# Kernel tuning notes

Measured on AMD Instinct MI355X. Metric: run time of the kernel, lower is better.

The kernel has to match this reference:

```python
import jax, jax.numpy as jnp
import numpy as np

N_NODES = 50000
N_EDGES = 800000
DIM = 256
DEPTH = 4
N_REL = 4
EPS = 1e-5


def setup_inputs() -> dict:
    key = jax.random.key(0)
    ks = jax.random.split(key, 8)
    scale = 1.0 / np.sqrt(DIM)
    return {
        "node_embedding": jax.random.normal(ks[0], (N_NODES, DIM), jnp.float32),
        "weights": jax.random.normal(ks[1], (DEPTH, N_REL, DIM, DIM), jnp.float32) * scale,
        "roots": jax.random.normal(ks[2], (DEPTH, DIM, DIM), jnp.float32) * scale,
        "biases": jax.random.normal(ks[3], (DEPTH, DIM), jnp.float32) * 0.01,
        "ln_gamma": jnp.ones((DEPTH, DIM), jnp.float32),
        "ln_beta": jnp.zeros((DEPTH, DIM), jnp.float32),
        "edge_index": jax.random.randint(ks[4], (2, N_EDGES), 0, N_NODES, jnp.int32),
        "edge_type": jax.random.randint(ks[5], (N_EDGES,), 0, N_REL, jnp.int32),
    }


def _rgcn_layer(X, W, root, bias, gamma, beta, src, dst, etype, inv_deg):
    # RGCNConv with aggr='mean': per-relation transform, then per-relation mean
    # over incoming edges at the target node, summed across relations.
    h = jnp.einsum('ni,rio->rno', X, W)            # [R, N, D]
    msg = h[etype, src] * inv_deg[:, None]         # [E, D] gather + per-relation 1/deg
    agg = jax.ops.segment_sum(msg, dst, num_segments=X.shape[0])  # [N, D]
    out = agg + X @ root + bias
    # LayerNorm
    mu = jnp.mean(out, axis=-1, keepdims=True)
    var = jnp.mean(jnp.square(out - mu), axis=-1, keepdims=True)
    out = (out - mu) * jax.lax.rsqrt(var + EPS) * gamma + beta
    out = jax.nn.elu(out)
    return out + X  # residual connection (dropout p=0 -> identity)


def reference(node_embedding, weights, roots, biases, ln_gamma, ln_beta, edge_index, edge_type):
    src, dst = edge_index[0], edge_index[1]
    # per-(node, relation) in-degree for the relation-wise mean aggregation
    cnt = jnp.zeros((node_embedding.shape[0], N_REL), node_embedding.dtype)
    cnt = cnt.at[dst, edge_type].add(1.0)
    inv_deg = 1.0 / jnp.maximum(cnt[dst, edge_type], 1.0)  # [E]
    X = node_embedding
    for l in range(DEPTH):
        X = _rgcn_layer(X, weights[l], roots[l], biases[l], ln_gamma[l], ln_beta[l],
                        src, dst, edge_type, inv_deg)
    return X
```

## Files before the change

kernel.cpp:

```cpp
#include <hip/hip_runtime.h>
#include <hip/hip_bf16.h>
#include <stdint.h>

#define NN 50000
#define NE 800000
#define DD 256
#define NL 4
#define NRL 4
#define KT 1280
#define KA 1024

typedef float f32x4 __attribute__((ext_vector_type(4)));
typedef __bf16 bf16x8 __attribute__((ext_vector_type(8)));
typedef __bf16 bf16x4 __attribute__((ext_vector_type(4)));
typedef unsigned short u16x4 __attribute__((ext_vector_type(4)));

static __device__ __forceinline__ unsigned short f2bf(float f) {
  __bf16 h = (__bf16)f;
  return __builtin_bit_cast(unsigned short, h);
}

static __device__ __forceinline__ u16x4 pk4(f32x4 v) {
  u16x4 o;
  o.x = f2bf(v.x); o.y = f2bf(v.y); o.z = f2bf(v.z); o.w = f2bf(v.w);
  return o;
}

static __device__ __forceinline__ void async16(const void* g, void* l) {
  __builtin_amdgcn_global_load_lds(
      (const __attribute__((address_space(1))) unsigned int*)g,
      (__attribute__((address_space(3))) unsigned int*)l, 16, 0, 0);
}

static __device__ __forceinline__ void async16nt(const void* g, void* l) {
  __builtin_amdgcn_global_load_lds(
      (const __attribute__((address_space(1))) unsigned int*)g,
      (__attribute__((address_space(3))) unsigned int*)l, 16, 0, 2);
}


__global__ __launch_bounds__(256) void k_hist(const int* __restrict__ ei,
                                              const int* __restrict__ et,
                                              int* __restrict__ cntNR) {
  int e = blockIdx.x * 256 + threadIdx.x;
  if (e >= NE) return;
  int dst = ei[NE + e];
  int r = et[e];
  atomicAdd(&cntNR[dst * 4 + r], 1);
}

__global__ __launch_bounds__(256) void k_scan1(const int* __restrict__ cntNR,
                                               int* __restrict__ offs,
                                               int* __restrict__ bsum) {
  __shared__ int sd[256];
  const int t = threadIdx.x;
  const int n = blockIdx.x * 256 + t;
  int deg = 0;
  if (n < NN) {
    const int* c = cntNR + n * 4;
    deg = c[0] + c[1] + c[2] + c[3];
  }
  sd[t] = deg;
  __syncthreads();
  int val = deg;
  for (int d = 1; d < 256; d <<= 1) {
    int other = (t >= d) ? sd[t - d] : 0;
    __syncthreads();
    val += other;
    sd[t] = val;
    __syncthreads();
  }
  if (n < NN) offs[n] = val - deg;
  if (t == 255) bsum[blockIdx.x] = val;
}

__global__ __launch_bounds__(256) void k_scan2(const int* __restrict__ bsum,
                                               int* __restrict__ boff, int nb) {
  __shared__ int sd[256];
  const int t = threadIdx.x;
  int v = (t < nb) ? bsum[t] : 0;
  sd[t] = v;
  __syncthreads();
  int val = v;
  for (int d = 1; d < 256; d <<= 1) {
    int other = (t >= d) ? sd[t - d] : 0;
    __syncthreads();
    val += other;
    sd[t] = val;
    __syncthreads();
  }
  boff[t] = val - v;
}

__global__ __launch_bounds__(256) void k_scan3(int* __restrict__ offs,
                                               const int* __restrict__ boff,
                                               int* __restrict__ cursor) {
  int n = blockIdx.x * 256 + threadIdx.x;
  if (n < NN) {
    int o = offs[n] + boff[blockIdx.x];
    offs[n] = o;
    cursor[n] = o;
  }
  if (n == 0) offs[NN] = NE;
}

__global__ __launch_bounds__(256) void k_scatter(const int* __restrict__ ei,
                                                 const int* __restrict__ et,
                                                 int* __restrict__ cursor,
                                                 uint32_t* __restrict__ packed) {
  int e = blockIdx.x * 256 + threadIdx.x;
  if (e >= NE) return;
  int src = ei[e];
  int dst = ei[NE + e];
  int r = et[e];
  int pos = atomicAdd(&cursor[dst], 1);
  packed[pos] = (uint32_t)src | ((uint32_t)r << 16);
}

__global__ __launch_bounds__(256) void k_wconv(const float* __restrict__ weights,
                                               const float* __restrict__ roots,
                                               __hip_bfloat16* __restrict__ WbigT) {
  int idx = blockIdx.x * 256 + threadIdx.x;
  if (idx >= NL * DD * KT) return;
  int l = idx / (DD * KT);
  int rem = idx - l * (DD * KT);
  int o = rem / KT;
  int k = rem - o * KT;
  float v;
  if (k < NRL * DD) {
    int r = k >> 8, i = k & 255;
    v = weights[(((size_t)(l * NRL + r) * DD) + i) * DD + o];
  } else {
    int i = k - NRL * DD;
    v = roots[((size_t)l * DD + i) * DD + o];
  }
  WbigT[idx] = __float2bfloat16(v);
}

__global__ __launch_bounds__(256) void k_cast(const float* __restrict__ X,
                                              __hip_bfloat16* __restrict__ Xbf) {
  int i = blockIdx.x * 256 + threadIdx.x;
  if (i >= NN * 64) return;
  const f32x4* Xv = (const f32x4*)X;
  ((u16x4*)Xbf)[i] = pk4(Xv[i]);
}


__global__ __launch_bounds__(256) void k_agg(const __hip_bfloat16* __restrict__ Xbf,
                                             const uint32_t* __restrict__ packed,
                                             const int* __restrict__ offs,
                                             const int* __restrict__ cntNR,
                                             __hip_bfloat16* __restrict__ Abig) {
  const int wid = (blockIdx.x * 256 + threadIdx.x) >> 6;
  const int lane = threadIdx.x & 63;
  if (wid >= NN) return;
  const int beg = offs[wid];
  const int end = offs[wid + 1];
  const bf16x4* __restrict__ Xv = (const bf16x4*)Xbf;

  f32x4 a0 = {0.f, 0.f, 0.f, 0.f}, a1 = a0, a2 = a0, a3 = a0;

  for (int e = beg; e < end; e += 8) {
    uint32_t pv[8];
    bf16x4 vv[8];
#pragma unroll
    for (int i = 0; i < 8; ++i) {
      int ee = e + i;
      ee = (ee < end) ? ee : (end - 1);
      pv[i] = packed[ee];
    }
#pragma unroll
    for (int i = 0; i < 8; ++i) {
      vv[i] = Xv[(int)(pv[i] & 0xFFFFu) * 64 + lane];
    }
    const int nv = end - e;
#pragma unroll
    for (int i = 0; i < 8; ++i) {
      if (i < nv) {
        int r = (int)(pv[i] >> 16);
        f32x4 v = {(float)vv[i][0], (float)vv[i][1], (float)vv[i][2], (float)vv[i][3]};
        if (r == 0) a0 += v;
        else if (r == 1) a1 += v;
        else if (r == 2) a2 += v;
        else a3 += v;
      }
    }
  }

  const int* c = cntNR + wid * 4;
  int c0 = c[0], c1 = c[1], c2 = c[2], c3 = c[3];
  float s0 = 1.0f / (float)(c0 > 1 ? c0 : 1);
  float s1 = 1.0f / (float)(c1 > 1 ? c1 : 1);
  float s2 = 1.0f / (float)(c2 > 1 ? c2 : 1);
  float s3 = 1.0f / (float)(c3 > 1 ? c3 : 1);

  u16x4* Arow = (u16x4*)(Abig + (size_t)wid * KA);
  __builtin_nontemporal_store(pk4(a0 * s0), Arow + 0 * 64 + lane);
  __builtin_nontemporal_store(pk4(a1 * s1), Arow + 1 * 64 + lane);
  __builtin_nontemporal_store(pk4(a2 * s2), Arow + 2 * 64 + lane);
  __builtin_nontemporal_store(pk4(a3 * s3), Arow + 3 * 64 + lane);
}


#define GBUF 20480
#define NTILE 40

__global__ __launch_bounds__(256, 2) void k_gemm(const __hip_bfloat16* __restrict__ A,
                                                 const __hip_bfloat16* __restrict__ Xbf_in,
                                                 const __hip_bfloat16* __restrict__ Bt,
                                                 const float* __restrict__ bias,
                                                 const float* __restrict__ gamma,
                                                 const float* __restrict__ beta,
                                                 const float* __restrict__ Xin,
                                                 float* __restrict__ Xout,
                                                 __hip_bfloat16* __restrict__ Xbf_out) {
  __shared__ __align__(16) char sLDS[3 * GBUF];
  __shared__ float sRed[64][4];

  const int tid = threadIdx.x;
  const int w = tid >> 6;
  const int lane = tid & 63;
  const int wm = w >> 1, wn = w & 1;
  const int quad = lane >> 4, l15 = lane & 15;
  const int mBase = blockIdx.x * 64;

  const int srow = lane >> 2;
  const int kc = (lane & 3) ^ ((srow >> 1) & 3);

  int am = mBase + w * 16 + srow;
  if (am >= NN) am = NN - 1;
  const char* agp = (const char*)A + (size_t)am * (KA * 2) + kc * 16;
  const char* agx = (const char*)Xbf_in + (size_t)am * (DD * 2) + kc * 16;
  const char* bgp0 = (const char*)Bt + (size_t)(w * 64 + 0 + srow) * (KT * 2) + kc * 16;
  const char* bgp1 = (const char*)Bt + (size_t)(w * 64 + 16 + srow) * (KT * 2) + kc * 16;
  const char* bgp2 = (const char*)Bt + (size_t)(w * 64 + 32 + srow) * (KT * 2) + kc * 16;
  const char* bgp3 = (const char*)Bt + (size_t)(w * 64 + 48 + srow) * (KT * 2) + kc * 16;

  char* const lA = sLDS + w * 1024;
  char* const lB = sLDS + 4096 + w * 4096;

  f32x4 acc[2][8];
#pragma unroll
  for (int i = 0; i < 2; ++i)
#pragma unroll
    for (int j = 0; j < 8; ++j) acc[i][j] = (f32x4){0.f, 0.f, 0.f, 0.f};

  const int aslot = (quad ^ ((l15 >> 1) & 3)) * 16;
  const char* const aBase = sLDS + (wm * 32 + l15) * 64 + aslot;
  const char* const bBase = sLDS + 4096 + (wn * 128 + l15) * 64 + aslot;

  auto STAGE = [&](int buf, int ts) {
    const int k0 = ts * 64;
    char* la = lA + buf * GBUF;
    char* lb = lB + buf * GBUF;
    if (k0 < KA * 2) {
      async16nt(agp + k0, la);
    } else {
      async16(agx + (k0 - KA * 2), la);
    }
    async16(bgp0 + k0, lb);
    async16(bgp1 + k0, lb + 1024);
    async16(bgp2 + k0, lb + 2048);
    async16(bgp3 + k0, lb + 3072);
  };

  STAGE(0, 0);
  int cb = 0, sb = 1;
  for (int t = 0; t < NTILE; ++t) {
    const int ts = (t + 1 < NTILE) ? (t + 1) : (NTILE - 1);
    STAGE(sb, ts);
    __builtin_amdgcn_sched_barrier(0);
    asm volatile("s_waitcnt vmcnt(5)" ::: "memory");
    __builtin_amdgcn_s_barrier();
    __builtin_amdgcn_sched_barrier(0);

    const char* aAddr = aBase + cb * GBUF;
    const char* bAddr = bBase + cb * GBUF;
    bf16x8 a0 = *(const bf16x8*)(aAddr + 0 * 1024);
    bf16x8 a1 = *(const bf16x8*)(aAddr + 1 * 1024);
#pragma unroll
    for (int nt = 0; nt < 8; ++nt) {
      bf16x8 b = *(const bf16x8*)(bAddr + nt * 1024);
      acc[0][nt] = __builtin_amdgcn_mfma_f32_16x16x32_bf16(a0, b, acc[0][nt], 0, 0, 0);
      acc[1][nt] = __builtin_amdgcn_mfma_f32_16x16x32_bf16(a1, b, acc[1][nt], 0, 0, 0);
    }
    cb = (cb == 2) ? 0 : cb + 1;
    sb = (sb == 2) ? 0 : sb + 1;
  }

  float bv[8], gv[8], bev[8];
#pragma unroll
  for (int nt = 0; nt < 8; ++nt) {
    int n = wn * 128 + nt * 16 + l15;
    bv[nt] = bias[n];
    gv[nt] = gamma[n];
    bev[nt] = beta[n];
  }

#pragma unroll
  for (int mt = 0; mt < 2; ++mt) {
#pragma unroll
    for (int reg = 0; reg < 4; ++reg) {
      float s = 0.f, q = 0.f;
#pragma unroll
      for (int nt = 0; nt < 8; ++nt) {
        float v = acc[mt][nt][reg] + bv[nt];
        acc[mt][nt][reg] = v;
        s += v;
        q += v * v;
      }
#pragma unroll
      for (int d = 1; d < 16; d <<= 1) {
        s += __shfl_xor(s, d, 64);
        q += __shfl_xor(q, d, 64);
      }
      if (l15 == 0) {
        int row = wm * 32 + mt * 16 + quad * 4 + reg;
        sRed[row][wn * 2] = s;
        sRed[row][wn * 2 + 1] = q;
      }
    }
  }
  __syncthreads();

#pragma unroll
  for (int mt = 0; mt < 2; ++mt) {
#pragma unroll
    for (int reg = 0; reg < 4; ++reg) {
      int row = wm * 32 + mt * 16 + quad * 4 + reg;
      float ts = sRed[row][0] + sRed[row][2];
      float tq = sRed[row][1] + sRed[row][3];
      float mean = ts * (1.0f / 256.0f);
      float var = tq * (1.0f / 256.0f) - mean * mean;
      float rstd = rsqrtf(var + 1e-5f);
      int m = mBase + row;
      if (m < NN) {
#pragma unroll
        for (int nt = 0; nt < 8; ++nt) {
          int n = wn * 128 + nt * 16 + l15;
          float v = (acc[mt][nt][reg] - mean) * rstd * gv[nt] + bev[nt];
          v = v > 0.0f ? v : (__expf(v) - 1.0f);
          float res = v + Xin[(size_t)m * 256 + n];
          Xout[(size_t)m * 256 + n] = res;
          Xbf_out[(size_t)m * 256 + n] = __float2bfloat16(res);
        }
      }
    }
  }
}


extern "C" void kernel_launch(void* const* d_in, const int* in_sizes, int n_in,
                              void* d_out, int out_size, void* d_ws, size_t ws_size,
                              hipStream_t stream) {
  const float* X0 = (const float*)d_in[0];
  const float* weights = (const float*)d_in[1];
  const float* roots = (const float*)d_in[2];
  const float* biases = (const float*)d_in[3];
  const float* ln_g = (const float*)d_in[4];
  const float* ln_b = (const float*)d_in[5];
  const int* eidx = (const int*)d_in[6];
  const int* etyp = (const int*)d_in[7];
  float* out = (float*)d_out;

  char* ws = (char*)d_ws;
  size_t off = 0;
  auto alloc = [&](size_t bytes) -> char* {
    char* p = ws + off;
    off = (off + bytes + 255) & ~(size_t)255;
    return p;
  };
  __hip_bfloat16* Abig = (__hip_bfloat16*)alloc((size_t)NN * KA * 2);
  __hip_bfloat16* WbigT = (__hip_bfloat16*)alloc((size_t)NL * DD * KT * 2);
  float* Xb0 = (float*)alloc((size_t)NN * DD * 4);
  float* Xb1 = (float*)alloc((size_t)NN * DD * 4);
  __hip_bfloat16* Xbf0 = (__hip_bfloat16*)alloc((size_t)NN * DD * 2);
  __hip_bfloat16* Xbf1 = (__hip_bfloat16*)alloc((size_t)NN * DD * 2);
  int* cntNR = (int*)alloc((size_t)NN * 4 * 4);
  int* offs = (int*)alloc((size_t)(NN + 1) * 4);
  int* cursor = (int*)alloc((size_t)NN * 4);
  uint32_t* packed = (uint32_t*)alloc((size_t)NE * 4);
  int* bsum = (int*)alloc(256 * 4);
  int* boff = (int*)alloc(256 * 4);
  (void)ws_size; (void)in_sizes; (void)n_in; (void)out_size;

  (void)hipMemsetAsync(cntNR, 0, (size_t)NN * 16, stream);
  k_hist<<<(NE + 255) / 256, 256, 0, stream>>>(eidx, etyp, cntNR);
  const int NB = (NN + 255) / 256;
  k_scan1<<<NB, 256, 0, stream>>>(cntNR, offs, bsum);
  k_scan2<<<1, 256, 0, stream>>>(bsum, boff, NB);
  k_scan3<<<NB, 256, 0, stream>>>(offs, boff, cursor);
  k_scatter<<<(NE + 255) / 256, 256, 0, stream>>>(eidx, etyp, cursor, packed);
  k_wconv<<<(NL * DD * KT + 255) / 256, 256, 0, stream>>>(weights, roots, WbigT);
  k_cast<<<(NN * 64 + 255) / 256, 256, 0, stream>>>(X0, Xbf0);

  const float* Xin = X0;
  for (int l = 0; l < NL; ++l) {
    float* Xout = (l == NL - 1) ? out : ((l & 1) ? Xb1 : Xb0);
    const __hip_bfloat16* Xbin = (l & 1) ? Xbf1 : Xbf0;
    __hip_bfloat16* Xbout = (l & 1) ? Xbf0 : Xbf1;
    k_agg<<<(NN * 64 + 255) / 256, 256, 0, stream>>>(Xbin, packed, offs, cntNR, Abig);
    k_gemm<<<(NN + 63) / 64, 256, 0, stream>>>(Abig, Xbin,
                                               WbigT + (size_t)l * DD * KT,
                                               biases + (size_t)l * DD,
                                               ln_g + (size_t)l * DD,
                                               ln_b + (size_t)l * DD, Xin, Xout, Xbout);
    Xin = Xout;
  }
}
```

Baseline: 970.9 us.

## Deepen GEMM LDS pipeline to four buffers and retune cache hints

The GEMM's async global-to-LDS pipeline grows from three buffers with one tile in flight to four buffers with two tiles prefetched ahead, plus explicit drain iterations at the end. The aim is to hide more global-load latency behind the MFMA work. The LayerNorm reduction scratch now reuses the pipeline LDS after a __syncthreads, so total LDS only grows by about one buffer. Cache hints also move: the aggregate matrix A is now written and loaded as ordinary cached traffic, while the fp32 residual read and output write become nontemporal. The larger LDS footprint (about 80KB per block) may limit how many blocks fit per CU.

```diff
diff --git a/kernel.cpp b/kernel.cpp
--- a/kernel.cpp
+++ b/kernel.cpp
@@ -30,12 +30,6 @@
   __builtin_amdgcn_global_load_lds(
       (const __attribute__((address_space(1))) unsigned int*)g,
       (__attribute__((address_space(3))) unsigned int*)l, 16, 0, 0);
-}
-
-static __device__ __forceinline__ void async16nt(const void* g, void* l) {
-  __builtin_amdgcn_global_load_lds(
-      (const __attribute__((address_space(1))) unsigned int*)g,
-      (__attribute__((address_space(3))) unsigned int*)l, 16, 0, 2);
 }
 
 
@@ -195,10 +189,10 @@
   float s3 = 1.0f / (float)(c3 > 1 ? c3 : 1);
 
   u16x4* Arow = (u16x4*)(Abig + (size_t)wid * KA);
-  __builtin_nontemporal_store(pk4(a0 * s0), Arow + 0 * 64 + lane);
-  __builtin_nontemporal_store(pk4(a1 * s1), Arow + 1 * 64 + lane);
-  __builtin_nontemporal_store(pk4(a2 * s2), Arow + 2 * 64 + lane);
-  __builtin_nontemporal_store(pk4(a3 * s3), Arow + 3 * 64 + lane);
+  Arow[0 * 64 + lane] = pk4(a0 * s0);
+  Arow[1 * 64 + lane] = pk4(a1 * s1);
+  Arow[2 * 64 + lane] = pk4(a2 * s2);
+  Arow[3 * 64 + lane] = pk4(a3 * s3);
 }
 
 
@@ -214,8 +208,8 @@
                                                  const float* __restrict__ Xin,
                                                  float* __restrict__ Xout,
                                                  __hip_bfloat16* __restrict__ Xbf_out) {
-  __shared__ __align__(16) char sLDS[3 * GBUF];
-  __shared__ float sRed[64][4];
+  __shared__ __align__(16) char sLDS[4 * GBUF];
+  float(*sRed)[4] = (float(*)[4])sLDS;
 
   const int tid = threadIdx.x;
   const int w = tid >> 6;
@@ -254,7 +248,7 @@
     char* la = lA + buf * GBUF;
     char* lb = lB + buf * GBUF;
     if (k0 < KA * 2) {
-      async16nt(agp + k0, la);
+      async16(agp + k0, la);
     } else {
       async16(agx + (k0 - KA * 2), la);
     }
@@ -264,18 +258,9 @@
     async16(bgp3 + k0, lb + 3072);
   };
 
-  STAGE(0, 0);
-  int cb = 0, sb = 1;
-  for (int t = 0; t < NTILE; ++t) {
-    const int ts = (t + 1 < NTILE) ? (t + 1) : (NTILE - 1);
-    STAGE(sb, ts);
-    __builtin_amdgcn_sched_barrier(0);
-    asm volatile("s_waitcnt vmcnt(5)" ::: "memory");
-    __builtin_amdgcn_s_barrier();
-    __builtin_amdgcn_sched_barrier(0);
-
-    const char* aAddr = aBase + cb * GBUF;
-    const char* bAddr = bBase + cb * GBUF;
+  auto COMPUTE = [&](int buf) {
+    const char* aAddr = aBase + buf * GBUF;
+    const char* bAddr = bBase + buf * GBUF;
     bf16x8 a0 = *(const bf16x8*)(aAddr + 0 * 1024);
     bf16x8 a1 = *(const bf16x8*)(aAddr + 1 * 1024);
 #pragma unroll
@@ -284,9 +269,32 @@
       acc[0][nt] = __builtin_amdgcn_mfma_f32_16x16x32_bf16(a0, b, acc[0][nt], 0, 0, 0);
       acc[1][nt] = __builtin_amdgcn_mfma_f32_16x16x32_bf16(a1, b, acc[1][nt], 0, 0, 0);
     }
-    cb = (cb == 2) ? 0 : cb + 1;
-    sb = (sb == 2) ? 0 : sb + 1;
-  }
+  };
+
+  STAGE(0, 0);
+  STAGE(1, 1);
+  int cb = 0, sb = 2;
+  for (int t = 0; t < NTILE - 2; ++t) {
+    STAGE(sb, t + 2);
+    __builtin_amdgcn_sched_barrier(0);
+    asm volatile("s_waitcnt vmcnt(10)" ::: "memory");
+    __builtin_amdgcn_s_barrier();
+    __builtin_amdgcn_sched_barrier(0);
+    COMPUTE(cb);
+    cb = (cb + 1) & 3;
+    sb = (sb + 1) & 3;
+  }
+  asm volatile("s_waitcnt vmcnt(5)" ::: "memory");
+  __builtin_amdgcn_s_barrier();
+  __builtin_amdgcn_sched_barrier(0);
+  COMPUTE(cb);
+  cb = (cb + 1) & 3;
+  asm volatile("s_waitcnt vmcnt(0)" ::: "memory");
+  __builtin_amdgcn_s_barrier();
+  __builtin_amdgcn_sched_barrier(0);
+  COMPUTE(cb);
+
+  __syncthreads();
 
   float bv[8], gv[8], bev[8];
 #pragma unroll
@@ -340,8 +348,8 @@
           int n = wn * 128 + nt * 16 + l15;
           float v = (acc[mt][nt][reg] - mean) * rstd * gv[nt] + bev[nt];
           v = v > 0.0f ? v : (__expf(v) - 1.0f);
-          float res = v + Xin[(size_t)m * 256 + n];
-          Xout[(size_t)m * 256 + n] = res;
+          float res = v + __builtin_nontemporal_load(&Xin[(size_t)m * 256 + n]);
+          __builtin_nontemporal_store(res, &Xout[(size_t)m * 256 + n]);
           Xbf_out[(size_t)m * 256 + n] = __float2bfloat16(res);
         }
       }
```

Result: faster. 866.4 us (-10.8%).
